# Performance work log

Measured on AMD Instinct MI355X. Metric: run time of the kernel, lower is better.

Reference implementation:

```python
import jax, jax.numpy as jnp
import numpy as np

EMBED_DIM = 1024
WINDOW = 256
NUM_HEADS = 16
HEAD_DIM = EMBED_DIM // NUM_HEADS
SCALE = HEAD_DIM ** (-0.5)


def setup_inputs() -> dict:
    key = jax.random.key(0)
    ks = jax.random.split(key, 9)
    B, S, E = 4, 4096, EMBED_DIM
    std = E ** (-0.5)
    x = jax.random.normal(ks[0], (B, S, E), dtype=jnp.float32)
    Wq = jax.random.normal(ks[1], (E, E), dtype=jnp.float32) * std
    Wk = jax.random.normal(ks[2], (E, E), dtype=jnp.float32) * std
    Wv = jax.random.normal(ks[3], (E, E), dtype=jnp.float32) * std
    Wo = jax.random.normal(ks[4], (E, E), dtype=jnp.float32) * std
    bq = jax.random.normal(ks[5], (E,), dtype=jnp.float32) * 0.01
    bk = jax.random.normal(ks[6], (E,), dtype=jnp.float32) * 0.01
    bv = jax.random.normal(ks[7], (E,), dtype=jnp.float32) * 0.01
    bo = jax.random.normal(ks[8], (E,), dtype=jnp.float32) * 0.01
    return {"x": x, "Wq": Wq, "bq": bq, "Wk": Wk, "bk": bk,
            "Wv": Wv, "bv": bv, "Wo": Wo, "bo": bo}


def reference(x, Wq, bq, Wk, bk, Wv, bv, Wo, bo):
    B, S, E = x.shape
    W = WINDOW
    nw = S // W  # seq_len chosen divisible by window_size
    # projections (torch Linear: x @ W.T + b); no head split in the original
    q = x @ Wq.T + bq
    k = x @ Wk.T + bk
    v = x @ Wv.T + bv
    # split into non-overlapping windows: [B, nw, W, E]
    qw = q.reshape(B, nw, W, E)
    kw = k.reshape(B, nw, W, E)
    vw = v.reshape(B, nw, W, E)
    scores = jnp.einsum('bnqe,bnke->bnqk', qw, kw) * SCALE  # [B, nw, W, W]
    causal = jnp.tril(jnp.ones((W, W), dtype=bool))
    scores = jnp.where(causal, scores, -jnp.inf)
    attn = jax.nn.softmax(scores, axis=-1)
    out = jnp.einsum('bnqk,bnke->bnqe', attn, vw).reshape(B, S, E)
    out = out @ Wo.T + bo
    return out + x
```

## Files before the change

### kernel.cpp

```cpp
#include <hip/hip_runtime.h>
#include <hip/hip_bf16.h>


typedef unsigned short u16;
typedef __attribute__((ext_vector_type(8))) short short8;
typedef __attribute__((ext_vector_type(4))) short short4v;
typedef __attribute__((ext_vector_type(4))) float f32x4;

__device__ __forceinline__ u16 f2bf(float f) {
    __hip_bfloat16 h = __float2bfloat16(f);
    return __builtin_bit_cast(u16, h);
}

__global__ void prep(const float* __restrict__ x, u16* __restrict__ xb,
                     const float* __restrict__ Wq, const float* __restrict__ Wk,
                     const float* __restrict__ Wv, const float* __restrict__ Wo,
                     u16* __restrict__ WqT, u16* __restrict__ WkT,
                     u16* __restrict__ WvT, u16* __restrict__ Wob,
                     const float* __restrict__ bq, const float* __restrict__ bv,
                     const float* __restrict__ bo,
                     float* __restrict__ u, float* __restrict__ b2)
{
    __shared__ float lt[64][65];
    const int t = threadIdx.x;
    const int blk = blockIdx.x;
    if (blk < 8192) {
        int i = (blk * 256 + t) * 8;
        const float4* s = (const float4*)(x + i);
        float4 a = s[0], b = s[1];
        short8 o;
        o[0] = (short)f2bf(a.x); o[1] = (short)f2bf(a.y); o[2] = (short)f2bf(a.z); o[3] = (short)f2bf(a.w);
        o[4] = (short)f2bf(b.x); o[5] = (short)f2bf(b.y); o[6] = (short)f2bf(b.z); o[7] = (short)f2bf(b.w);
        *(short8*)(xb + i) = o;
        return;
    }
    if (blk < 9216) {
        const int wb = blk - 8192;
        const int which = wb >> 8;
        const int bid = wb & 255;
        const int c0 = (bid & 15) * 64, r0 = (bid >> 4) * 64;
        const int tr = t >> 3, tc = (t & 7) * 8;
        const float* src = which == 0 ? Wq : which == 1 ? Wk : which == 2 ? Wv : Wo;
        if (which == 3) {
#pragma unroll
            for (int p = 0; p < 2; ++p) {
                int r = p * 32 + tr;
                const float* s = src + (size_t)(r0 + r) * 1024 + c0 + tc;
                float4 a = *(const float4*)s, b = *(const float4*)(s + 4);
                short8 o;
                o[0] = (short)f2bf(a.x); o[1] = (short)f2bf(a.y); o[2] = (short)f2bf(a.z); o[3] = (short)f2bf(a.w);
                o[4] = (short)f2bf(b.x); o[5] = (short)f2bf(b.y); o[6] = (short)f2bf(b.z); o[7] = (short)f2bf(b.w);
                *(short8*)(Wob + (size_t)(r0 + r) * 1024 + c0 + tc) = o;
            }
            return;
        }
        u16* dst = which == 0 ? WqT : which == 1 ? WkT : WvT;
#pragma unroll
        for (int p = 0; p < 2; ++p) {
            int r = p * 32 + tr;
            const float* s = src + (size_t)(r0 + r) * 1024 + c0 + tc;
            float4 a = *(const float4*)s, b = *(const float4*)(s + 4);
            lt[r][tc + 0] = a.x; lt[r][tc + 1] = a.y; lt[r][tc + 2] = a.z; lt[r][tc + 3] = a.w;
            lt[r][tc + 4] = b.x; lt[r][tc + 5] = b.y; lt[r][tc + 6] = b.z; lt[r][tc + 7] = b.w;
        }
        __syncthreads();
#pragma unroll
        for (int p = 0; p < 2; ++p) {
            int r = p * 32 + tr;
            short8 o;
#pragma unroll
            for (int j = 0; j < 8; ++j) o[j] = (short)f2bf(lt[tc + j][r]);
            *(short8*)(dst + (size_t)(c0 + r) * 1024 + r0 + tc) = o;
        }
        return;
    }
    {
        const int bid = blk - 9216;
        if (bid < 4) {
            int b = bid * 256 + t;
            float acc = 0.f;
            for (int o = 0; o < 1024; ++o) acc += Wk[(size_t)o * 1024 + b] * bq[o];
            u[b] = acc;
        } else {
            int n = (bid - 4) * 16 + (t >> 4);
            int l = t & 15;
            float acc = 0.f;
            for (int m = l; m < 1024; m += 16) acc += Wo[(size_t)n * 1024 + m] * bv[m];
#pragma unroll
            for (int s = 1; s < 16; s <<= 1) acc += __shfl_xor(acc, s, 64);
            if (l == 0) b2[n] = acc + bo[n];
        }
    }
}

__global__ __launch_bounds__(256, 4) void gemm_small_dual(
    const u16* __restrict__ HA, const u16* __restrict__ HB, u16* __restrict__ HC,
    const u16* __restrict__ WA, const u16* __restrict__ WB, u16* __restrict__ WC)
{
    __shared__ __align__(16) u16 At[64 * 64], Bt[64 * 64];
    const bool sec = blockIdx.x >= 256;
    const u16* A = sec ? WA : HA;
    const u16* B = sec ? WB : HB;
    u16* C = sec ? WC : HC;
    const int bid = blockIdx.x & 255;
    const int m0 = (bid >> 4) * 64, n0 = (bid & 15) * 64;
    const int t = threadIdx.x, lane = t & 63, w = t >> 6;
    const int l15 = lane & 15, lk = lane >> 4;

    f32x4 acc[4];
#pragma unroll
    for (int m = 0; m < 4; ++m) acc[m] = (f32x4){0.f, 0.f, 0.f, 0.f};

    for (int k0 = 0; k0 < 1024; k0 += 64) {
        __syncthreads();
#pragma unroll
        for (int p = 0; p < 2; ++p) {
            int e = p * 2048 + t * 8;
            int row = e >> 6, col = e & 63;
            short8 va = *(const short8*)(A + (size_t)(m0 + row) * 1024 + k0 + col);
            *(short8*)((char*)At + row * 128 + ((col * 2) ^ ((row & 7) << 4))) = va;
            short8 vb = *(const short8*)(B + (size_t)(n0 + row) * 1024 + k0 + col);
            *(short8*)((char*)Bt + row * 128 + ((col * 2) ^ ((row & 7) << 4))) = vb;
        }
        __syncthreads();
#pragma unroll
        for (int ks = 0; ks < 2; ++ks) {
            int bc = ks * 64 + lk * 16;
            int brow = w * 16 + l15;
            short8 bfr = *(const short8*)((char*)Bt + brow * 128 + (bc ^ ((brow & 7) << 4)));
#pragma unroll
            for (int m = 0; m < 4; ++m) {
                int arow = m * 16 + l15;
                short8 af = *(const short8*)((char*)At + arow * 128 + (bc ^ ((arow & 7) << 4)));
                acc[m] = __builtin_amdgcn_mfma_f32_16x16x32_bf16(af, bfr, acc[m], 0, 0, 0);
            }
        }
    }
#pragma unroll
    for (int m = 0; m < 4; ++m)
#pragma unroll
        for (int r = 0; r < 4; ++r) {
            int row = m0 + m * 16 + lk * 4 + r;
            int col = n0 + w * 16 + l15;
            C[(size_t)row * 1024 + col] = f2bf(acc[m][r]);
        }
}

__global__ __launch_bounds__(256, 2) void gemm_yv(
    const u16* __restrict__ A, const u16* __restrict__ BH, const u16* __restrict__ BW,
    const float* __restrict__ ub, u16* __restrict__ Y, u16* __restrict__ V2t)
{
    __shared__ __align__(16) u16 At[128 * 64];
    __shared__ __align__(16) u16 Bt[128 * 64];
    const int t = threadIdx.x;
    const int lane = t & 63;
    const int wid = t >> 6;
    const int wm = wid >> 1, wn = wid & 1;
    const int l15 = lane & 15, lk = lane >> 4;
    const int K = 1024;

    const int bid = blockIdx.y * gridDim.x + blockIdx.x;
    const int cpx = 2048 >> 3;
    const int swz = (bid & 7) * cpx + (bid >> 3);
    const int tn = swz & 15;
    const int tm = swz >> 4;
    const int m0 = tm * 128;
    const bool isv = tn >= 8;
    const int n0 = (tn & 7) * 128;
    const u16* B = isv ? BW : BH;

    f32x4 acc[4][4];
#pragma unroll
    for (int m = 0; m < 4; ++m)
#pragma unroll
        for (int n = 0; n < 4; ++n)
            acc[m][n] = (f32x4){0.f, 0.f, 0.f, 0.f};

    for (int k0 = 0; k0 < K; k0 += 64) {
        __syncthreads();
#pragma unroll
        for (int p = 0; p < 4; ++p) {
            int e = p * 2048 + t * 8;
            int row = e >> 6, col = e & 63;
            short8 va = *(const short8*)(A + (size_t)(m0 + row) * K + k0 + col);
            *(short8*)((char*)At + row * 128 + ((col * 2) ^ ((row & 7) << 4))) = va;
            short8 vb = *(const short8*)(B + (size_t)(n0 + row) * K + k0 + col);
            *(short8*)((char*)Bt + row * 128 + ((col * 2) ^ ((row & 7) << 4))) = vb;
        }
        __syncthreads();
#pragma unroll
        for (int ks = 0; ks < 2; ++ks) {
            const int bc = ks * 64 + lk * 16;
            short8 af[4], bfr[4];
#pragma unroll
            for (int m = 0; m < 4; ++m) {
                int row = wm * 64 + m * 16 + l15;
                af[m] = *(const short8*)((char*)At + row * 128 + (bc ^ ((row & 7) << 4)));
            }
#pragma unroll
            for (int n = 0; n < 4; ++n) {
                int row = wn * 64 + n * 16 + l15;
                bfr[n] = *(const short8*)((char*)Bt + row * 128 + (bc ^ ((row & 7) << 4)));
            }
#pragma unroll
            for (int m = 0; m < 4; ++m)
#pragma unroll
                for (int n = 0; n < 4; ++n)
                    acc[m][n] = __builtin_amdgcn_mfma_f32_16x16x32_bf16(af[m], bfr[n], acc[m][n], 0, 0, 0);
        }
    }

    if (!isv) {
#pragma unroll
        for (int m = 0; m < 4; ++m)
#pragma unroll
            for (int n = 0; n < 4; ++n) {
                int col = n0 + wn * 64 + n * 16 + l15;
                float bv = ub[col];
#pragma unroll
                for (int r = 0; r < 4; ++r) {
                    int row = m0 + wm * 64 + m * 16 + lk * 4 + r;
                    Y[(size_t)row * 1024 + col] = f2bf(acc[m][n][r] + bv);
                }
            }
    } else {
#pragma unroll
        for (int m = 0; m < 4; ++m)
#pragma unroll
            for (int n = 0; n < 4; ++n) {
                int col = n0 + wn * 64 + n * 16 + l15;
                int row0 = m0 + wm * 64 + m * 16 + lk * 4;
                short4v pk;
#pragma unroll
                for (int r = 0; r < 4; ++r) pk[r] = (short)f2bf(acc[m][n][r]);
                *(short4v*)(V2t + (size_t)col * 16384 + row0) = pk;
            }
    }
}

__global__ __launch_bounds__(256, 1) void attn_win(
    const u16* __restrict__ y, const u16* __restrict__ xb,
    const u16* __restrict__ vt, const float* __restrict__ xres,
    const float* __restrict__ b2, float* __restrict__ outp)
{
    __shared__ __align__(16) char smem[116736];
    u16* P  = (u16*)(smem + 81920);
    float* rmax = (float*)(smem + 114688);
    float* rsum = (float*)(smem + 115712);

    const int t = threadIdx.x;
    const int lane = t & 63, wv = t >> 6;
    const int l15 = lane & 15, lk = lane >> 4;
    const int bid = blockIdx.x;
    const int swz = (bid & 7) * 32 + (bid >> 3);
    const int win = swz >> 2, qc = swz & 3;
    const size_t qrow0 = (size_t)win * 256 + qc * 64;
    const size_t krow0 = (size_t)win * 256;

    f32x4 acc[4][4];
#pragma unroll
    for (int m = 0; m < 4; ++m)
#pragma unroll
        for (int n = 0; n < 4; ++n)
            acc[m][n] = (f32x4){0.f, 0.f, 0.f, 0.f};

    short8 pq[2], pk[8];
    auto LOAD_QK = [&](int e0) {
#pragma unroll
        for (int p = 0; p < 2; ++p) {
            int e = p * 2048 + t * 8;
            pq[p] = *(const short8*)(y + (qrow0 + (e >> 6)) * 1024 + e0 + (e & 63));
        }
#pragma unroll
        for (int p = 0; p < 8; ++p) {
            int e = p * 2048 + t * 8;
            pk[p] = *(const short8*)(xb + (krow0 + (e >> 6)) * 1024 + e0 + (e & 63));
        }
    };
    auto WRITE_QK = [&](int b) {
        char* Qt = smem + b * 40960;
        char* Kt = Qt + 8192;
#pragma unroll
        for (int p = 0; p < 2; ++p) {
            int e = p * 2048 + t * 8;
            int row = e >> 6, col = e & 63;
            *(short8*)(Qt + row * 128 + ((col * 2) ^ ((row & 7) << 4))) = pq[p];
        }
#pragma unroll
        for (int p = 0; p < 8; ++p) {
            int e = p * 2048 + t * 8;
            int row = e >> 6, col = e & 63;
            *(short8*)(Kt + row * 128 + ((col * 2) ^ ((row & 7) << 4))) = pk[p];
        }
    };

    LOAD_QK(0);
    WRITE_QK(0);
    LOAD_QK(64);
    __syncthreads();

    for (int i = 0; i < 16; ++i) {
        const int b = i & 1;
        if (i + 1 < 16) {
            WRITE_QK(b ^ 1);
            if (i + 2 < 16) LOAD_QK((i + 2) * 64);
        }
        const char* Qt = smem + b * 40960;
        const char* Kt = Qt + 8192;
#pragma unroll
        for (int ks = 0; ks < 2; ++ks) {
            const int bc = ks * 64 + lk * 16;
            short8 af[4], bfr[4];
#pragma unroll
            for (int m = 0; m < 4; ++m) {
                int row = m * 16 + l15;
                af[m] = *(const short8*)(Qt + row * 128 + (bc ^ ((row & 7) << 4)));
            }
#pragma unroll
            for (int n = 0; n < 4; ++n) {
                int row = wv * 64 + n * 16 + l15;
                bfr[n] = *(const short8*)(Kt + row * 128 + (bc ^ ((row & 7) << 4)));
            }
            __builtin_amdgcn_s_setprio(1);
#pragma unroll
            for (int m = 0; m < 4; ++m)
#pragma unroll
                for (int n = 0; n < 4; ++n)
                    acc[m][n] = __builtin_amdgcn_mfma_f32_16x16x32_bf16(af[m], bfr[n], acc[m][n], 0, 0, 0);
            __builtin_amdgcn_s_setprio(0);
        }
        __syncthreads();
    }

#pragma unroll
    for (int m = 0; m < 4; ++m)
#pragma unroll
        for (int n = 0; n < 4; ++n) {
            int col = wv * 64 + n * 16 + l15;
#pragma unroll
            for (int r = 0; r < 4; ++r) {
                int qpos = qc * 64 + m * 16 + lk * 4 + r;
                float v = acc[m][n][r] * 0.125f;
                acc[m][n][r] = (col <= qpos) ? v : -1e30f;
            }
        }
#pragma unroll
    for (int m = 0; m < 4; ++m)
#pragma unroll
        for (int r = 0; r < 4; ++r) {
            float tmx = fmaxf(fmaxf(acc[m][0][r], acc[m][1][r]), fmaxf(acc[m][2][r], acc[m][3][r]));
            tmx = fmaxf(tmx, __shfl_xor(tmx, 1));
            tmx = fmaxf(tmx, __shfl_xor(tmx, 2));
            tmx = fmaxf(tmx, __shfl_xor(tmx, 4));
            tmx = fmaxf(tmx, __shfl_xor(tmx, 8));
            if (l15 == 0) rmax[(m * 16 + lk * 4 + r) * 4 + wv] = tmx;
        }
    __syncthreads();
#pragma unroll
    for (int m = 0; m < 4; ++m)
#pragma unroll
        for (int r = 0; r < 4; ++r) {
            int row = m * 16 + lk * 4 + r;
            float m4 = fmaxf(fmaxf(rmax[row * 4], rmax[row * 4 + 1]),
                             fmaxf(rmax[row * 4 + 2], rmax[row * 4 + 3]));
            float s = 0.f;
#pragma unroll
            for (int n = 0; n < 4; ++n) {
                float e = __expf(acc[m][n][r] - m4);
                acc[m][n][r] = e;
                s += e;
            }
            s += __shfl_xor(s, 1);
            s += __shfl_xor(s, 2);
            s += __shfl_xor(s, 4);
            s += __shfl_xor(s, 8);
            if (l15 == 0) rsum[row * 4 + wv] = s;
        }
    __syncthreads();
#pragma unroll
    for (int m = 0; m < 4; ++m)
#pragma unroll
        for (int r = 0; r < 4; ++r) {
            int row = m * 16 + lk * 4 + r;
            float inv = 1.f / (rsum[row * 4] + rsum[row * 4 + 1] + rsum[row * 4 + 2] + rsum[row * 4 + 3]);
#pragma unroll
            for (int n = 0; n < 4; ++n) {
                int col = wv * 64 + n * 16 + l15;
                *(u16*)((char*)P + row * 512 + ((col * 2) ^ ((row & 7) << 4))) = f2bf(acc[m][n][r] * inv);
            }
        }

    short8 pv[8];
    auto LOAD_V = [&](int n0) {
#pragma unroll
        for (int p = 0; p < 8; ++p) {
            int e = p * 2048 + t * 8;
            pv[p] = *(const short8*)(vt + (size_t)(n0 + (e >> 8)) * 16384 + win * 256 + (e & 255));
        }
    };
    auto WRITE_V = [&](int b) {
        char* Vl = smem + b * 40960;
#pragma unroll
        for (int p = 0; p < 8; ++p) {
            int e = p * 2048 + t * 8;
            int row = e >> 8, col = e & 255;
            *(short8*)(Vl + row * 512 + ((col * 2) ^ ((row & 7) << 4))) = pv[p];
        }
    };

    LOAD_V(0);
    WRITE_V(0);
    LOAD_V(64);
    __syncthreads();

    for (int i = 0; i < 16; ++i) {
        const int b = i & 1;
        const int n0 = i * 64;
        if (i + 1 < 16) {
            WRITE_V(b ^ 1);
            if (i + 2 < 16) LOAD_V((i + 2) * 64);
        }
        const char* Vl = smem + b * 40960;
        f32x4 acc2[4];
#pragma unroll
        for (int m = 0; m < 4; ++m) acc2[m] = (f32x4){0.f, 0.f, 0.f, 0.f};
#pragma unroll
        for (int ks = 0; ks < 8; ++ks) {
            const int bc = ks * 64 + lk * 16;
            short8 af[4];
#pragma unroll
            for (int m = 0; m < 4; ++m) {
                int row = m * 16 + l15;
                af[m] = *(const short8*)((char*)P + row * 512 + (bc ^ ((row & 7) << 4)));
            }
            int vrow = wv * 16 + l15;
            short8 bfr = *(const short8*)(Vl + vrow * 512 + (bc ^ ((vrow & 7) << 4)));
            __builtin_amdgcn_s_setprio(1);
#pragma unroll
            for (int m = 0; m < 4; ++m)
                acc2[m] = __builtin_amdgcn_mfma_f32_16x16x32_bf16(af[m], bfr, acc2[m], 0, 0, 0);
            __builtin_amdgcn_s_setprio(0);
        }
#pragma unroll
        for (int m = 0; m < 4; ++m) {
#pragma unroll
            for (int r = 0; r < 4; ++r) {
                int row = m * 16 + lk * 4 + r;
                int col = n0 + wv * 16 + l15;
                size_t idx = (qrow0 + row) * 1024 + col;
                outp[idx] = acc2[m][r] + b2[col] + xres[idx];
            }
        }
        __syncthreads();
    }
}

extern "C" void kernel_launch(void* const* d_in, const int* in_sizes, int n_in,
                              void* d_out, int out_size, void* d_ws, size_t ws_size,
                              hipStream_t stream) {
    const float* x  = (const float*)d_in[0];
    const float* Wq = (const float*)d_in[1];
    const float* bq = (const float*)d_in[2];
    const float* Wk = (const float*)d_in[3];
    const float* Wv = (const float*)d_in[5];
    const float* bv = (const float*)d_in[6];
    const float* Wo = (const float*)d_in[7];
    const float* bo = (const float*)d_in[8];
    float* out = (float*)d_out;

    char* ws = (char*)d_ws;
    u16* xb  = (u16*)(ws);
    u16* yb  = (u16*)(ws + 33554432);
    u16* v2t = (u16*)(ws + 67108864);
    u16* WqT = (u16*)(ws + 100663296);
    u16* WkT = (u16*)(ws + 102760448);
    u16* WvT = (u16*)(ws + 104857600);
    u16* Wob = (u16*)(ws + 106954752);
    u16* Hb  = (u16*)(ws + 109051904);
    u16* W2b = (u16*)(ws + 111149056);
    float* u_  = (float*)(ws + 113246208);
    float* b2_ = (float*)(ws + 113250304);

    prep<<<9284, 256, 0, stream>>>(x, xb, Wq, Wk, Wv, Wo, WqT, WkT, WvT, Wob,
                                   bq, bv, bo, u_, b2_);
    gemm_small_dual<<<512, 256, 0, stream>>>(WkT, WqT, Hb, Wob, WvT, W2b);
    gemm_yv<<<dim3(16, 128), 256, 0, stream>>>(xb, Hb, W2b, u_, yb, v2t);
    attn_win<<<256, 256, 0, stream>>>(yb, xb, v2t, x, b2_, out);
}
```

Baseline: 197.9 us.

## Rewrite gemm_yv as 256x256 double-buffered GEMM with direct global-to-LDS loads

The main projection GEMM moves from 128x128 tiles with 4 waves and synchronous register-staged loads to 256x256 tiles with 8 waves. K-tiles are double-buffered in 128KB of LDS, filled through global_load_lds DMA, and interleaved with MFMA phases using explicit vmcnt waits, barriers and setprio. The goal is to hide global load latency, raise arithmetic intensity per block, and skip the register round-trip for staging. In exchange it holds 128 accumulator registers per thread and allows only one block per CU with 512 blocks. The hand-written waitcnt and barrier schedule is fragile if the load counts are wrong.

```diff
diff --git a/kernel.cpp b/kernel.cpp
--- a/kernel.cpp
+++ b/kernel.cpp
@@ -10,6 +10,13 @@
 __device__ __forceinline__ u16 f2bf(float f) {
     __hip_bfloat16 h = __float2bfloat16(f);
     return __builtin_bit_cast(u16, h);
+}
+
+__device__ __forceinline__ void gl_lds16(const u16* g, u16* l) {
+    __builtin_amdgcn_global_load_lds(
+        (const __attribute__((address_space(1))) void*)g,
+        (__attribute__((address_space(3))) void*)l,
+        16, 0, 0);
 }
 
 __global__ void prep(const float* __restrict__ x, u16* __restrict__ xb,
@@ -146,93 +153,148 @@
         }
 }
 
-__global__ __launch_bounds__(256, 2) void gemm_yv(
+__global__ __launch_bounds__(512) void gemm_yv(
     const u16* __restrict__ A, const u16* __restrict__ BH, const u16* __restrict__ BW,
     const float* __restrict__ ub, u16* __restrict__ Y, u16* __restrict__ V2t)
 {
-    __shared__ __align__(16) u16 At[128 * 64];
-    __shared__ __align__(16) u16 Bt[128 * 64];
+    __shared__ __align__(16) char smbuf[131072];
+    char* A0 = smbuf;
+    char* B0 = smbuf + 32768;
+    char* A1 = smbuf + 65536;
+    char* B1 = smbuf + 98304;
+
     const int t = threadIdx.x;
-    const int lane = t & 63;
-    const int wid = t >> 6;
-    const int wm = wid >> 1, wn = wid & 1;
+    const int lane = t & 63, w = t >> 6;
     const int l15 = lane & 15, lk = lane >> 4;
+    const int wm = w >> 2, wn = w & 3;
     const int K = 1024;
 
-    const int bid = blockIdx.y * gridDim.x + blockIdx.x;
-    const int cpx = 2048 >> 3;
-    const int swz = (bid & 7) * cpx + (bid >> 3);
-    const int tn = swz & 15;
-    const int tm = swz >> 4;
-    const int m0 = tm * 128;
-    const bool isv = tn >= 8;
-    const int n0 = (tn & 7) * 128;
+    const int bid = blockIdx.y * 8 + blockIdx.x;
+    const int swz = (bid & 7) * 64 + (bid >> 3);
+    const int tn = swz & 7, tm = swz >> 3;
+    const int m0 = tm * 256;
+    const bool isv = tn >= 4;
+    const int n0 = (tn & 3) * 256;
     const u16* B = isv ? BW : BH;
 
-    f32x4 acc[4][4];
-#pragma unroll
-    for (int m = 0; m < 4; ++m)
-#pragma unroll
-        for (int n = 0; n < 4; ++n)
-            acc[m][n] = (f32x4){0.f, 0.f, 0.f, 0.f};
-
-    for (int k0 = 0; k0 < K; k0 += 64) {
-        __syncthreads();
-#pragma unroll
-        for (int p = 0; p < 4; ++p) {
-            int e = p * 2048 + t * 8;
-            int row = e >> 6, col = e & 63;
-            short8 va = *(const short8*)(A + (size_t)(m0 + row) * K + k0 + col);
-            *(short8*)((char*)At + row * 128 + ((col * 2) ^ ((row & 7) << 4))) = va;
-            short8 vb = *(const short8*)(B + (size_t)(n0 + row) * K + k0 + col);
-            *(short8*)((char*)Bt + row * 128 + ((col * 2) ^ ((row & 7) << 4))) = vb;
-        }
-        __syncthreads();
-#pragma unroll
-        for (int ks = 0; ks < 2; ++ks) {
-            const int bc = ks * 64 + lk * 16;
-            short8 af[4], bfr[4];
-#pragma unroll
-            for (int m = 0; m < 4; ++m) {
-                int row = wm * 64 + m * 16 + l15;
-                af[m] = *(const short8*)((char*)At + row * 128 + (bc ^ ((row & 7) << 4)));
-            }
-#pragma unroll
-            for (int n = 0; n < 4; ++n) {
-                int row = wn * 64 + n * 16 + l15;
-                bfr[n] = *(const short8*)((char*)Bt + row * 128 + (bc ^ ((row & 7) << 4)));
-            }
-#pragma unroll
-            for (int m = 0; m < 4; ++m)
-#pragma unroll
-                for (int n = 0; n < 4; ++n)
-                    acc[m][n] = __builtin_amdgcn_mfma_f32_16x16x32_bf16(af[m], bfr[n], acc[m][n], 0, 0, 0);
-        }
+    const int srow = t >> 3;
+    const int scg = ((t & 7) ^ (srow & 7)) * 8;
+
+    f32x4 acc[8][4];
+#pragma unroll
+    for (int mf = 0; mf < 8; ++mf)
+#pragma unroll
+        for (int nf = 0; nf < 4; ++nf)
+            acc[mf][nf] = (f32x4){0.f, 0.f, 0.f, 0.f};
+
+    auto STAGE_T = [&](const u16* G, int gr0, int k0, char* dst) {
+#pragma unroll
+        for (int h = 0; h < 2; ++h)
+#pragma unroll
+            for (int c = 0; c < 2; ++c) {
+                int ri = h * 128 + c * 64 + srow;
+                gl_lds16(G + (size_t)(gr0 + ri) * K + k0 + scg,
+                         (u16*)(dst + h * 16384 + c * 8192 + t * 16));
+            }
+    };
+    auto RD = [&](const char* tile, int r, int kc) -> short8 {
+        return *(const short8*)(tile + r * 128 + ((kc ^ (r & 7)) << 4));
+    };
+
+    short8 av[4], bv[4];
+    auto LA = [&](const char* tA, int mfb, int ks) {
+#pragma unroll
+        for (int f = 0; f < 4; ++f)
+            av[f] = RD(tA, wm * 128 + (mfb + f) * 16 + l15, ks * 4 + lk);
+    };
+    auto LB = [&](const char* tB, int ks) {
+#pragma unroll
+        for (int f = 0; f < 4; ++f)
+            bv[f] = RD(tB, wn * 64 + f * 16 + l15, ks * 4 + lk);
+    };
+    auto MM = [&](int mfb) {
+        __builtin_amdgcn_s_setprio(1);
+#pragma unroll
+        for (int f = 0; f < 4; ++f)
+#pragma unroll
+            for (int nf = 0; nf < 4; ++nf)
+                acc[mfb + f][nf] = __builtin_amdgcn_mfma_f32_16x16x32_bf16(av[f], bv[nf], acc[mfb + f][nf], 0, 0, 0);
+        __builtin_amdgcn_s_setprio(0);
+    };
+    auto BARW = [&] {
+        __builtin_amdgcn_s_barrier();
+        asm volatile("s_waitcnt lgkmcnt(0)" ::: "memory");
+        __builtin_amdgcn_sched_barrier(0);
+    };
+    auto BARE = [&] {
+        __builtin_amdgcn_s_barrier();
+        __builtin_amdgcn_sched_barrier(0);
+    };
+
+    STAGE_T(A, m0, 0, A0);
+    STAGE_T(B, n0, 0, B0);
+    STAGE_T(A, m0, 64, A1);
+    STAGE_T(B, n0, 64, B1);
+    asm volatile("s_waitcnt vmcnt(8)" ::: "memory");
+    __builtin_amdgcn_s_barrier();
+    __builtin_amdgcn_sched_barrier(0);
+
+    for (int j = 0; j < 8; ++j) {
+        LA(A0, 0, 0); LB(B0, 0);
+        if (j >= 1) STAGE_T(A, m0, (2 * j + 1) * 64, A1);
+        BARW(); MM(0); BARE();
+        LA(A0, 4, 0);
+        BARW(); MM(4); BARE();
+        LA(A0, 0, 1); LB(B0, 1);
+        BARW(); MM(0); BARE();
+        LA(A0, 4, 1);
+        if (2 * j + 2 < 16) {
+            STAGE_T(B, n0, (2 * j + 2) * 64, B0);
+            asm volatile("s_waitcnt vmcnt(4)" ::: "memory");
+        } else {
+            asm volatile("s_waitcnt vmcnt(0)" ::: "memory");
+        }
+        BARW(); MM(4); BARE();
+        LA(A1, 0, 0); LB(B1, 0);
+        if (2 * j + 2 < 16) STAGE_T(A, m0, (2 * j + 2) * 64, A0);
+        BARW(); MM(0); BARE();
+        LA(A1, 4, 0);
+        BARW(); MM(4); BARE();
+        LA(A1, 0, 1); LB(B1, 1);
+        BARW(); MM(0); BARE();
+        LA(A1, 4, 1);
+        if (2 * j + 3 < 16) {
+            STAGE_T(B, n0, (2 * j + 3) * 64, B1);
+            asm volatile("s_waitcnt vmcnt(4)" ::: "memory");
+        } else {
+            asm volatile("s_waitcnt vmcnt(0)" ::: "memory");
+        }
+        BARW(); MM(4); BARE();
     }
 
     if (!isv) {
 #pragma unroll
-        for (int m = 0; m < 4; ++m)
-#pragma unroll
-            for (int n = 0; n < 4; ++n) {
-                int col = n0 + wn * 64 + n * 16 + l15;
-                float bv = ub[col];
+        for (int mf = 0; mf < 8; ++mf)
+#pragma unroll
+            for (int nf = 0; nf < 4; ++nf) {
+                int col = n0 + wn * 64 + nf * 16 + l15;
+                float bvx = ub[col];
 #pragma unroll
                 for (int r = 0; r < 4; ++r) {
-                    int row = m0 + wm * 64 + m * 16 + lk * 4 + r;
-                    Y[(size_t)row * 1024 + col] = f2bf(acc[m][n][r] + bv);
+                    int row = m0 + wm * 128 + mf * 16 + lk * 4 + r;
+                    Y[(size_t)row * 1024 + col] = f2bf(acc[mf][nf][r] + bvx);
                 }
             }
     } else {
 #pragma unroll
-        for (int m = 0; m < 4; ++m)
-#pragma unroll
-            for (int n = 0; n < 4; ++n) {
-                int col = n0 + wn * 64 + n * 16 + l15;
-                int row0 = m0 + wm * 64 + m * 16 + lk * 4;
+        for (int mf = 0; mf < 8; ++mf)
+#pragma unroll
+            for (int nf = 0; nf < 4; ++nf) {
+                int col = n0 + wn * 64 + nf * 16 + l15;
+                int row0 = m0 + wm * 128 + mf * 16 + lk * 4;
                 short4v pk;
 #pragma unroll
-                for (int r = 0; r < 4; ++r) pk[r] = (short)f2bf(acc[m][n][r]);
+                for (int r = 0; r < 4; ++r) pk[r] = (short)f2bf(acc[mf][nf][r]);
                 *(short4v*)(V2t + (size_t)col * 16384 + row0) = pk;
             }
     }
@@ -484,6 +546,6 @@
     prep<<<9284, 256, 0, stream>>>(x, xb, Wq, Wk, Wv, Wo, WqT, WkT, WvT, Wob,
                                    bq, bv, bo, u_, b2_);
     gemm_small_dual<<<512, 256, 0, stream>>>(WkT, WqT, Hb, Wob, WvT, W2b);
-    gemm_yv<<<dim3(16, 128), 256, 0, stream>>>(xb, Hb, W2b, u_, yb, v2t);
+    gemm_yv<<<dim3(8, 64), 512, 0, stream>>>(xb, Hb, W2b, u_, yb, v2t);
     attn_win<<<256, 256, 0, stream>>>(yb, xb, v2t, x, b2_, out);
 }
```

Result: no change. 199.4 us (+0.7%).
